# Optimization experiments

Hardware: AMD Instinct MI355X
Metric: run time of the kernel (lower is better)

Reference implementation:

```python
import jax, jax.numpy as jnp
import numpy as np

TEMPERATURE = 1.0
N_NODES = 50000
N_EDGES = 1600000
BATCH = 2
C_IN = 64
C_OUT = 64


def setup_inputs() -> dict:
    key = jax.random.key(0)
    k = jax.random.split(key, 8)
    # edge_index with no self-loops: tgt = (src + 1 + off) % N, off in [0, N-2)
    src = jax.random.randint(k[0], (N_EDGES,), 0, N_NODES, dtype=jnp.int64)
    off = jax.random.randint(k[1], (N_EDGES,), 0, N_NODES - 1, dtype=jnp.int64)
    tgt = (src + 1 + off) % N_NODES
    edge_index = jnp.stack([src, tgt])  # (2, E)
    x = jax.random.normal(k[2], (BATCH, N_NODES, C_IN), dtype=jnp.float32)
    f_disc_orig = jax.random.uniform(k[3], (N_EDGES,), dtype=jnp.float32)
    fluxes = jax.random.normal(k[4], (BATCH, N_NODES), dtype=jnp.float32)
    W_conc = jax.random.normal(k[5], (C_OUT, C_IN), dtype=jnp.float32) * (1.0 / np.sqrt(C_IN))
    W_disc = jax.random.normal(k[6], (C_OUT, C_IN), dtype=jnp.float32) * (1.0 / np.sqrt(C_IN))
    bias = jnp.zeros((C_OUT,), dtype=jnp.float32)
    return {"x": x, "edge_index": edge_index, "f_disc_orig": f_disc_orig,
            "fluxes": fluxes, "W_conc": W_conc, "W_disc": W_disc, "bias": bias}


def reference(x, edge_index, f_disc_orig, fluxes, W_conc, W_disc, bias):
    B, N, _ = x.shape
    src0, tgt0 = edge_index[0], edge_index[1]  # original edges (no self-loops)
    loops = jnp.arange(N, dtype=edge_index.dtype)
    src = jnp.concatenate([src0, loops])  # (E+N,)
    tgt = jnp.concatenate([tgt0, loops])
    # GCN symmetric normalization D^{-1/2} A D^{-1/2} (with self-loops)
    deg = jnp.zeros((N,), x.dtype).at[tgt].add(1.0)
    dis = jnp.where(deg > 0, jax.lax.rsqrt(jnp.maximum(deg, 1e-30)), 0.0)
    norm = dis[src] * dis[tgt]  # (E+N,)
    # dynamic discordant strength on original (non-self-loop) edges
    sign_prod = jnp.tanh(fluxes[:, src0] * fluxes[:, tgt0] / TEMPERATURE)  # (B, E)
    keep = (1.0 + sign_prod) * 0.5
    fdo = f_disc_orig[None, :]
    f_disc = keep * fdo + (1.0 - keep) * (1.0 - fdo)  # (B, E)
    # self-loop messages are purely concordant (f_disc = 0)
    f_full = jnp.concatenate([f_disc, jnp.zeros((B, N), x.dtype)], axis=1)  # (B, E+N)
    # transform once per node, then gather per edge
    xc = jnp.einsum('bni,oi->bno', x, W_conc)  # (B, N, O)
    xd = jnp.einsum('bni,oi->bno', x, W_disc)
    msg = norm[None, :, None] * ((1.0 - f_full)[..., None] * xc[:, src] +
                                 f_full[..., None] * xd[:, src])  # (B, E+N, O)
    out = jnp.zeros((B, N, xc.shape[-1]), x.dtype).at[:, tgt].add(msg)
    return out + bias
```

## Files before the change

### kernel.cpp

```cpp
#include <hip/hip_runtime.h>
#include <math.h>


constexpr int C = 64;
constexpr int CNB = 512;
constexpr int CCAP = 18432;

typedef short short8 __attribute__((ext_vector_type(8)));
typedef float f32x4 __attribute__((ext_vector_type(4)));

__device__ __forceinline__ unsigned pack_bf16x2(float a, float b) {
    unsigned ua = __float_as_uint(a);
    ua = (ua + 0x7fffu + ((ua >> 16) & 1u)) >> 16;
    unsigned ub = __float_as_uint(b);
    ub = (ub + 0x7fffu + ((ub >> 16) & 1u)) >> 16;
    return ua | (ub << 16);
}
__device__ __forceinline__ float bflo(unsigned p) { return __uint_as_float(p << 16); }
__device__ __forceinline__ float bfhi(unsigned p) { return __uint_as_float(p & 0xffff0000u); }

__global__ __launch_bounds__(256) void convert_kernel(
    const float* __restrict__ x, unsigned* __restrict__ xb2, int nwords) {
    int i = blockIdx.x * blockDim.x + threadIdx.x;
    int stride = gridDim.x * blockDim.x;
    const float2* x2 = (const float2*)x;
    for (int w = i; w < nwords; w += stride) {
        float2 xv = x2[w];
        xb2[w] = pack_bf16x2(xv.x, xv.y);
    }
}

__global__ __launch_bounds__(256) void binA1_kernel(
    const int* __restrict__ src, const int* __restrict__ tgt,
    const float* __restrict__ fdo, int* __restrict__ coarseCursor,
    unsigned long long* __restrict__ slab, int E, int ncoarse) {
    __shared__ int hcnt[128];
    __shared__ int hbase[128];
    const int tid = threadIdx.x;
    const int chunk0 = blockIdx.x * 4096;
    if (tid < 128) hcnt[tid] = 0;
    __syncthreads();
#pragma unroll
    for (int k = 0; k < 16; ++k) {
        int e = chunk0 + tid + k * 256;
        if (e < E) atomicAdd(&hcnt[tgt[e] >> 9], 1);
    }
    __syncthreads();
    if (tid < ncoarse) {
        int c = hcnt[tid];
        hbase[tid] = c ? atomicAdd(&coarseCursor[tid], c) : 0;
        hcnt[tid] = 0;
    }
    __syncthreads();
#pragma unroll
    for (int k = 0; k < 16; ++k) {
        int e = chunk0 + tid + k * 256;
        if (e < E) {
            int t = tgt[e];
            int b = t >> 9;
            int pos = hbase[b] + atomicAdd(&hcnt[b], 1);
            if (pos < CCAP) {
                unsigned q = (unsigned)(fdo[e] * 32767.0f + 0.5f);
                unsigned long long en = (unsigned long long)(unsigned)src[e]
                                      | ((unsigned long long)(unsigned)(t & 511) << 17)
                                      | ((unsigned long long)q << 26);
                slab[(size_t)b * CCAP + pos] = en;
            }
        }
    }
}

__global__ __launch_bounds__(1024) void binA2_kernel(
    const unsigned long long* __restrict__ slab,
    const int* __restrict__ coarseCursor, const float* __restrict__ flux,
    unsigned* __restrict__ epackFine, float4* __restrict__ nodeinfo,
    int N, int ncoarse) {
    const int b = blockIdx.x;
    const int tid = threadIdx.x;
    __shared__ int ncnt[CNB];
    __shared__ int nsc[CNB];
    __shared__ int ncur[CNB];
    int cnt = min(coarseCursor[b], CCAP);
    if (tid < CNB) { ncnt[tid] = 0; ncur[tid] = 0; }
    __syncthreads();
    const unsigned long long* sl = slab + (size_t)b * CCAP;
    for (int i = tid; i < cnt; i += 1024)
        atomicAdd(&ncnt[(int)((sl[i] >> 17) & 511)], 1);
    __syncthreads();
    if (tid < CNB) nsc[tid] = ncnt[tid];
    __syncthreads();
    for (int off = 1; off < CNB; off <<= 1) {
        int v = (tid < CNB && tid >= off) ? nsc[tid - off] : 0;
        __syncthreads();
        if (tid < CNB) nsc[tid] += v;
        __syncthreads();
    }
    for (int i = tid; i < cnt; i += 1024) {
        unsigned long long e = sl[i];
        int s = (int)(e & 0x1FFFFull);
        int tl = (int)((e >> 17) & 511);
        unsigned q = (unsigned)((e >> 26) & 0x7FFF);
        int pos = nsc[tl] - ncnt[tl] + atomicAdd(&ncur[tl], 1);
        epackFine[(size_t)b * CCAP + pos] = (unsigned)s | (q << 17);
    }
    if (tid < CNB) {
        int n = b * CNB + tid;
        if (n < N) {
            int dg = ncnt[tid];
            int rs = b * CCAP + (nsc[tid] - dg);
            float4 ni;
            ni.x = rsqrtf((float)(dg + 1));
            ni.y = flux[n];
            ni.z = flux[N + n];
            ni.w = __int_as_float((dg << 21) | rs);
            nodeinfo[n] = ni;
        }
    }
}

__global__ __launch_bounds__(256) void aggregate_kernel(
    const float4* __restrict__ nodeinfo, const unsigned* __restrict__ epackFine,
    const unsigned* __restrict__ xb2, unsigned* __restrict__ up,
    unsigned* __restrict__ vp, int N) {
    const int lane = threadIdx.x & 63;
    const int wslot = threadIdx.x >> 6;
    const int node = blockIdx.x * 4 + wslot;
    __shared__ float4 s_e[4][2][64];
    if (node >= N) return;
    const int g = lane >> 5;
    const int hl = lane & 31;
    float4 ni = nodeinfo[node];
    const unsigned wbits = (unsigned)__float_as_int(ni.w);
    const int start = (int)(wbits & 0x1FFFFFu);
    const int end = start + (int)(wbits >> 21);
    const float dt = ni.x, f0t = ni.y, f1t = ni.z;
    const char* xbg = (const char*)xb2 + (size_t)g * N * 128 + hl * 4;
    float ux = 0.f, uy = 0.f, vx = 0.f, vy = 0.f;
    for (int base = start; base < end; base += 64) {
        int cnt64 = min(64, end - base);
        if (lane < cnt64) {
            unsigned p = epackFine[base + lane];
            int s = (int)(p & 0x1FFFFu);
            float fd = (float)(p >> 17) * (1.0f / 32767.0f);
            float4 nis = nodeinfo[s];
            float nrm = nis.x * dt;
            float p0 = nis.y * f0t;
            float p1 = nis.z * f1t;
            float k0 = 1.0f / (1.0f + __expf(-2.0f * p0));
            float k1 = 1.0f / (1.0f + __expf(-2.0f * p1));
            float w = 2.0f * fd - 1.0f;
            float f0 = fmaf(k0, w, 1.0f - fd);
            float f1 = fmaf(k1, w, 1.0f - fd);
            float soff = __int_as_float(s << 7);
            s_e[wslot][0][lane] = make_float4(soff, nrm * (1.0f - f0), nrm * f0, 0.f);
            s_e[wslot][1][lane] = make_float4(soff, nrm * (1.0f - f1), nrm * f1, 0.f);
        }
        float4 r = s_e[wslot][g][0];
        unsigned xpN = *(const unsigned*)(xbg + __float_as_int(r.x));
        float ccN = r.y, cdN = r.z;
        for (int j = 1; j < cnt64; ++j) {
            unsigned xp = xpN;
            float cc = ccN, cd = cdN;
            float4 r2 = s_e[wslot][g][j];
            xpN = *(const unsigned*)(xbg + __float_as_int(r2.x));
            ccN = r2.y; cdN = r2.z;
            float x0 = bflo(xp), x1 = bfhi(xp);
            ux = fmaf(cc, x0, ux); uy = fmaf(cc, x1, uy);
            vx = fmaf(cd, x0, vx); vy = fmaf(cd, x1, vy);
        }
        float x0 = bflo(xpN), x1 = bfhi(xpN);
        ux = fmaf(ccN, x0, ux); uy = fmaf(ccN, x1, uy);
        vx = fmaf(cdN, x0, vx); vy = fmaf(cdN, x1, vy);
    }
    unsigned xs = *(const unsigned*)(xbg + ((size_t)node << 7));
    float d2 = dt * dt;
    ux = fmaf(d2, bflo(xs), ux);
    uy = fmaf(d2, bfhi(xs), uy);
    size_t o32 = ((size_t)(g * N + node)) * 32 + hl;
    up[o32] = pack_bf16x2(ux, uy);
    vp[o32] = pack_bf16x2(vx, vy);
}

__device__ __forceinline__ short8 make_bfrag(const float* __restrict__ row, int off) {
    const float4* p = (const float4*)(row + off);
    float4 lo = p[0], hi = p[1];
    uint4 w;
    w.x = pack_bf16x2(lo.x, lo.y);
    w.y = pack_bf16x2(lo.z, lo.w);
    w.z = pack_bf16x2(hi.x, hi.y);
    w.w = pack_bf16x2(hi.z, hi.w);
    return __builtin_bit_cast(short8, w);
}

__global__ __launch_bounds__(256) void gemm_mfma_kernel(
    const unsigned* __restrict__ up, const unsigned* __restrict__ vp,
    const float* __restrict__ Wc, const float* __restrict__ Wd,
    const float* __restrict__ bias, float* __restrict__ out, int ntiles) {
    const int lane = threadIdx.x & 63;
    const int nl = lane & 15;
    const int quad = lane >> 4;
    const int wave = blockIdx.x * 4 + (threadIdx.x >> 6);
    const int nwaves = gridDim.x * 4;

    short8 bf[4][4];
    float bt[4];
#pragma unroll
    for (int t = 0; t < 4; ++t) {
        int n = 16 * t + nl;
        const float* wcr = Wc + n * 64;
        const float* wdr = Wd + n * 64;
        bf[0][t] = make_bfrag(wcr, quad * 8);
        bf[1][t] = make_bfrag(wcr, 32 + quad * 8);
        bf[2][t] = make_bfrag(wdr, quad * 8);
        bf[3][t] = make_bfrag(wdr, 32 + quad * 8);
        bt[t] = bias[n];
    }

    for (int tile = wave; tile < ntiles; tile += nwaves) {
        int row = tile * 16 + nl;
        const uint4* ur = (const uint4*)(up + (size_t)row * 32);
        const uint4* vr = (const uint4*)(vp + (size_t)row * 32);
        short8 a0 = __builtin_bit_cast(short8, ur[quad]);
        short8 a1 = __builtin_bit_cast(short8, ur[4 + quad]);
        short8 a2 = __builtin_bit_cast(short8, vr[quad]);
        short8 a3 = __builtin_bit_cast(short8, vr[4 + quad]);
        f32x4 acc[4];
#pragma unroll
        for (int t = 0; t < 4; ++t) {
            f32x4 z = {0.f, 0.f, 0.f, 0.f};
            acc[t] = __builtin_amdgcn_mfma_f32_16x16x32_bf16(a0, bf[0][t], z, 0, 0, 0);
            acc[t] = __builtin_amdgcn_mfma_f32_16x16x32_bf16(a1, bf[1][t], acc[t], 0, 0, 0);
            acc[t] = __builtin_amdgcn_mfma_f32_16x16x32_bf16(a2, bf[2][t], acc[t], 0, 0, 0);
            acc[t] = __builtin_amdgcn_mfma_f32_16x16x32_bf16(a3, bf[3][t], acc[t], 0, 0, 0);
        }
        float* ob = out + ((size_t)(tile * 16 + quad * 4) << 6);
#pragma unroll
        for (int t = 0; t < 4; ++t) {
            int col = 16 * t + nl;
#pragma unroll
            for (int r = 0; r < 4; ++r)
                ob[(r << 6) + col] = acc[t][r] + bt[t];
        }
    }
}

extern "C" void kernel_launch(void* const* d_in, const int* in_sizes, int n_in,
                              void* d_out, int out_size, void* d_ws, size_t ws_size,
                              hipStream_t stream) {
    const float* x = (const float*)d_in[0];
    const int* ei = (const int*)d_in[1];
    const float* fdo = (const float*)d_in[2];
    const float* flux = (const float*)d_in[3];
    const float* Wc = (const float*)d_in[4];
    const float* Wd = (const float*)d_in[5];
    const float* bias = (const float*)d_in[6];
    float* out = (float*)d_out;

    const int E = in_sizes[2];
    const int BN = in_sizes[3];
    const int N = BN / 2;
    const int ncoarse = (N + CNB - 1) / CNB;

    auto align = [](size_t o) { return (o + 255) & ~(size_t)255; };
    char* ws = (char*)d_ws;
    size_t o = 0;
    int* coarseCursor = (int*)(ws + o);
    size_t zero_end = align((size_t)ncoarse * 4);
    o = zero_end;
    float4* nodeinfo = (float4*)(ws + o);          o = align(o + (size_t)N * 16);
    unsigned long long* slab = (unsigned long long*)(ws + o);
    unsigned* up = (unsigned*)slab;
    o = align(o + (size_t)ncoarse * CCAP * 8);
    unsigned* epackFine = (unsigned*)(ws + o);     o = align(o + (size_t)ncoarse * CCAP * 4);
    unsigned* xb2 = (unsigned*)(ws + o);           o = align(o + (size_t)BN * 32 * 4);
    unsigned* vp = (unsigned*)(ws + o);            o += (size_t)BN * 32 * 4;

    const int* srcp = ei;
    const int* tgtp = ei + E;

    hipMemsetAsync(coarseCursor, 0, zero_end, stream);
    convert_kernel<<<2048, 256, 0, stream>>>(x, xb2, BN * 32);
    binA1_kernel<<<(E + 4095) / 4096, 256, 0, stream>>>(srcp, tgtp, fdo,
                                                        coarseCursor, slab, E, ncoarse);
    binA2_kernel<<<ncoarse, 1024, 0, stream>>>(slab, coarseCursor, flux,
                                               epackFine, nodeinfo, N, ncoarse);
    aggregate_kernel<<<(N + 3) / 4, 256, 0, stream>>>(nodeinfo, epackFine, xb2,
                                                      up, vp, N);
    gemm_mfma_kernel<<<512, 256, 0, stream>>>(up, vp, Wc, Wd, bias, out, BN / 16);
}
```

Before: 221.9 us.

## Widen aggregate gathers to 16B per lane, shrink coarse bins, fold memset

The aggregate kernel now processes four edges at a time per wavefront. Each 16-lane group loads 16-byte bf16 chunks of a source row, and the partial sums are reduced with cross-lane shuffles. This replaces 4-byte per-lane gathers, cutting the number of memory instructions and the length of the serial edge loop. Coarse bins shrink from 512 to 128 nodes, which gives more binA2 blocks, and binA1 handles larger chunks with a larger shared histogram. The cursor memset is folded into the convert kernel, but convert and binA1 both modify coarseCursor and ordering between them relies on stream order. CCAP=5120 for 128 nodes gives less per-bin headroom and risks overflow with skewed degrees.

New measurement: 220.7 us. Within noise of the previous version (-0.5%).

```diff
diff --git a/kernel.cpp b/kernel.cpp
--- a/kernel.cpp
+++ b/kernel.cpp
@@ -3,8 +3,8 @@
 
 
 constexpr int C = 64;
-constexpr int CNB = 512;
-constexpr int CCAP = 18432;
+constexpr int CNB = 128;
+constexpr int CCAP = 5120;
 
 typedef short short8 __attribute__((ext_vector_type(8)));
 typedef float f32x4 __attribute__((ext_vector_type(4)));
@@ -20,8 +20,10 @@
 __device__ __forceinline__ float bfhi(unsigned p) { return __uint_as_float(p & 0xffff0000u); }
 
 __global__ __launch_bounds__(256) void convert_kernel(
-    const float* __restrict__ x, unsigned* __restrict__ xb2, int nwords) {
+    const float* __restrict__ x, unsigned* __restrict__ xb2, int nwords,
+    int* __restrict__ coarseCursor, int ncoarse) {
     int i = blockIdx.x * blockDim.x + threadIdx.x;
+    if (i < ncoarse) coarseCursor[i] = 0;
     int stride = gridDim.x * blockDim.x;
     const float2* x2 = (const float2*)x;
     for (int w = i; w < nwords; w += stride) {
@@ -34,36 +36,36 @@
     const int* __restrict__ src, const int* __restrict__ tgt,
     const float* __restrict__ fdo, int* __restrict__ coarseCursor,
     unsigned long long* __restrict__ slab, int E, int ncoarse) {
-    __shared__ int hcnt[128];
-    __shared__ int hbase[128];
+    __shared__ int hcnt[512];
+    __shared__ int hbase[512];
     const int tid = threadIdx.x;
-    const int chunk0 = blockIdx.x * 4096;
-    if (tid < 128) hcnt[tid] = 0;
-    __syncthreads();
-#pragma unroll
-    for (int k = 0; k < 16; ++k) {
+    const int chunk0 = blockIdx.x * 8192;
+    for (int c = tid; c < 512; c += 256) hcnt[c] = 0;
+    __syncthreads();
+#pragma unroll 4
+    for (int k = 0; k < 32; ++k) {
         int e = chunk0 + tid + k * 256;
-        if (e < E) atomicAdd(&hcnt[tgt[e] >> 9], 1);
-    }
-    __syncthreads();
-    if (tid < ncoarse) {
-        int c = hcnt[tid];
-        hbase[tid] = c ? atomicAdd(&coarseCursor[tid], c) : 0;
-        hcnt[tid] = 0;
-    }
-    __syncthreads();
-#pragma unroll
-    for (int k = 0; k < 16; ++k) {
+        if (e < E) atomicAdd(&hcnt[tgt[e] >> 7], 1);
+    }
+    __syncthreads();
+    for (int c = tid; c < ncoarse; c += 256) {
+        int cc = hcnt[c];
+        hbase[c] = cc ? atomicAdd(&coarseCursor[c], cc) : 0;
+        hcnt[c] = 0;
+    }
+    __syncthreads();
+#pragma unroll 4
+    for (int k = 0; k < 32; ++k) {
         int e = chunk0 + tid + k * 256;
         if (e < E) {
             int t = tgt[e];
-            int b = t >> 9;
+            int b = t >> 7;
             int pos = hbase[b] + atomicAdd(&hcnt[b], 1);
             if (pos < CCAP) {
                 unsigned q = (unsigned)(fdo[e] * 32767.0f + 0.5f);
                 unsigned long long en = (unsigned long long)(unsigned)src[e]
-                                      | ((unsigned long long)(unsigned)(t & 511) << 17)
-                                      | ((unsigned long long)q << 26);
+                                      | ((unsigned long long)(unsigned)(t & 127) << 17)
+                                      | ((unsigned long long)q << 24);
                 slab[(size_t)b * CCAP + pos] = en;
             }
         }
@@ -73,8 +75,7 @@
 __global__ __launch_bounds__(1024) void binA2_kernel(
     const unsigned long long* __restrict__ slab,
     const int* __restrict__ coarseCursor, const float* __restrict__ flux,
-    unsigned* __restrict__ epackFine, float4* __restrict__ nodeinfo,
-    int N, int ncoarse) {
+    unsigned* __restrict__ epackFine, float4* __restrict__ nodeinfo, int N) {
     const int b = blockIdx.x;
     const int tid = threadIdx.x;
     __shared__ int ncnt[CNB];
@@ -85,7 +86,7 @@
     __syncthreads();
     const unsigned long long* sl = slab + (size_t)b * CCAP;
     for (int i = tid; i < cnt; i += 1024)
-        atomicAdd(&ncnt[(int)((sl[i] >> 17) & 511)], 1);
+        atomicAdd(&ncnt[(int)((sl[i] >> 17) & 127)], 1);
     __syncthreads();
     if (tid < CNB) nsc[tid] = ncnt[tid];
     __syncthreads();
@@ -98,8 +99,8 @@
     for (int i = tid; i < cnt; i += 1024) {
         unsigned long long e = sl[i];
         int s = (int)(e & 0x1FFFFull);
-        int tl = (int)((e >> 17) & 511);
-        unsigned q = (unsigned)((e >> 26) & 0x7FFF);
+        int tl = (int)((e >> 17) & 127);
+        unsigned q = (unsigned)((e >> 24) & 0x7FFF);
         int pos = nsc[tl] - ncnt[tl] + atomicAdd(&ncur[tl], 1);
         epackFine[(size_t)b * CCAP + pos] = (unsigned)s | (q << 17);
     }
@@ -127,21 +128,25 @@
     const int node = blockIdx.x * 4 + wslot;
     __shared__ float4 s_e[4][2][64];
     if (node >= N) return;
-    const int g = lane >> 5;
-    const int hl = lane & 31;
+    const int e2 = lane >> 4;
+    const int q16 = lane & 15;
+    const int g = q16 >> 3;
+    const int p = q16 & 7;
     float4 ni = nodeinfo[node];
     const unsigned wbits = (unsigned)__float_as_int(ni.w);
     const int start = (int)(wbits & 0x1FFFFFu);
     const int end = start + (int)(wbits >> 21);
     const float dt = ni.x, f0t = ni.y, f1t = ni.z;
-    const char* xbg = (const char*)xb2 + (size_t)g * N * 128 + hl * 4;
-    float ux = 0.f, uy = 0.f, vx = 0.f, vy = 0.f;
+    const char* xbg = (const char*)xb2 + (size_t)g * N * 128 + p * 16;
+    float au[8] = {0, 0, 0, 0, 0, 0, 0, 0};
+    float av[8] = {0, 0, 0, 0, 0, 0, 0, 0};
     for (int base = start; base < end; base += 64) {
-        int cnt64 = min(64, end - base);
-        if (lane < cnt64) {
-            unsigned p = epackFine[base + lane];
-            int s = (int)(p & 0x1FFFFu);
-            float fd = (float)(p >> 17) * (1.0f / 32767.0f);
+        int cnt = min(64, end - base);
+        int cntp = (cnt + 3) & ~3;
+        if (lane < cnt) {
+            unsigned pe = epackFine[base + lane];
+            int s = (int)(pe & 0x1FFFFu);
+            float fd = (float)(pe >> 17) * (1.0f / 32767.0f);
             float4 nis = nodeinfo[s];
             float nrm = nis.x * dt;
             float p0 = nis.y * f0t;
@@ -154,31 +159,69 @@
             float soff = __int_as_float(s << 7);
             s_e[wslot][0][lane] = make_float4(soff, nrm * (1.0f - f0), nrm * f0, 0.f);
             s_e[wslot][1][lane] = make_float4(soff, nrm * (1.0f - f1), nrm * f1, 0.f);
-        }
-        float4 r = s_e[wslot][g][0];
-        unsigned xpN = *(const unsigned*)(xbg + __float_as_int(r.x));
-        float ccN = r.y, cdN = r.z;
-        for (int j = 1; j < cnt64; ++j) {
-            unsigned xp = xpN;
+        } else if (lane < cntp) {
+            float4 z = make_float4(0.f, 0.f, 0.f, 0.f);
+            s_e[wslot][0][lane] = z;
+            s_e[wslot][1][lane] = z;
+        }
+        float4 r0 = s_e[wslot][g][e2];
+        uint4 xwN = *(const uint4*)(xbg + __float_as_int(r0.x));
+        float ccN = r0.y, cdN = r0.z;
+        for (int j = 4; j < cntp; j += 4) {
+            uint4 xw = xwN;
             float cc = ccN, cd = cdN;
-            float4 r2 = s_e[wslot][g][j];
-            xpN = *(const unsigned*)(xbg + __float_as_int(r2.x));
+            float4 r2 = s_e[wslot][g][j + e2];
+            xwN = *(const uint4*)(xbg + __float_as_int(r2.x));
             ccN = r2.y; cdN = r2.z;
-            float x0 = bflo(xp), x1 = bfhi(xp);
-            ux = fmaf(cc, x0, ux); uy = fmaf(cc, x1, uy);
-            vx = fmaf(cd, x0, vx); vy = fmaf(cd, x1, vy);
-        }
-        float x0 = bflo(xpN), x1 = bfhi(xpN);
-        ux = fmaf(ccN, x0, ux); uy = fmaf(ccN, x1, uy);
-        vx = fmaf(cdN, x0, vx); vy = fmaf(cdN, x1, vy);
-    }
-    unsigned xs = *(const unsigned*)(xbg + ((size_t)node << 7));
-    float d2 = dt * dt;
-    ux = fmaf(d2, bflo(xs), ux);
-    uy = fmaf(d2, bfhi(xs), uy);
-    size_t o32 = ((size_t)(g * N + node)) * 32 + hl;
-    up[o32] = pack_bf16x2(ux, uy);
-    vp[o32] = pack_bf16x2(vx, vy);
+#pragma unroll
+            for (int w = 0; w < 4; ++w) {
+                unsigned xp = (&xw.x)[w];
+                float lo = bflo(xp), hi = bfhi(xp);
+                au[2 * w] = fmaf(cc, lo, au[2 * w]);
+                au[2 * w + 1] = fmaf(cc, hi, au[2 * w + 1]);
+                av[2 * w] = fmaf(cd, lo, av[2 * w]);
+                av[2 * w + 1] = fmaf(cd, hi, av[2 * w + 1]);
+            }
+        }
+#pragma unroll
+        for (int w = 0; w < 4; ++w) {
+            unsigned xp = (&xwN.x)[w];
+            float lo = bflo(xp), hi = bfhi(xp);
+            au[2 * w] = fmaf(ccN, lo, au[2 * w]);
+            au[2 * w + 1] = fmaf(ccN, hi, au[2 * w + 1]);
+            av[2 * w] = fmaf(cdN, lo, av[2 * w]);
+            av[2 * w + 1] = fmaf(cdN, hi, av[2 * w + 1]);
+        }
+    }
+#pragma unroll
+    for (int k = 0; k < 8; ++k) {
+        au[k] += __shfl_xor(au[k], 16, 64);
+        au[k] += __shfl_xor(au[k], 32, 64);
+        av[k] += __shfl_xor(av[k], 16, 64);
+        av[k] += __shfl_xor(av[k], 32, 64);
+    }
+    if (e2 == 0) {
+        uint4 xs = *(const uint4*)(xbg + ((size_t)node << 7));
+        float d2 = dt * dt;
+#pragma unroll
+        for (int w = 0; w < 4; ++w) {
+            unsigned xp = (&xs.x)[w];
+            au[2 * w] = fmaf(d2, bflo(xp), au[2 * w]);
+            au[2 * w + 1] = fmaf(d2, bfhi(xp), au[2 * w + 1]);
+        }
+        uint4 uo, vo;
+        uo.x = pack_bf16x2(au[0], au[1]);
+        uo.y = pack_bf16x2(au[2], au[3]);
+        uo.z = pack_bf16x2(au[4], au[5]);
+        uo.w = pack_bf16x2(au[6], au[7]);
+        vo.x = pack_bf16x2(av[0], av[1]);
+        vo.y = pack_bf16x2(av[2], av[3]);
+        vo.z = pack_bf16x2(av[4], av[5]);
+        vo.w = pack_bf16x2(av[6], av[7]);
+        size_t wo = ((size_t)(g * N + node)) * 32 + 4 * p;
+        *(uint4*)(up + wo) = uo;
+        *(uint4*)(vp + wo) = vo;
+    }
 }
 
 __device__ __forceinline__ short8 make_bfrag(const float* __restrict__ row, int off) {
@@ -264,9 +307,7 @@
     auto align = [](size_t o) { return (o + 255) & ~(size_t)255; };
     char* ws = (char*)d_ws;
     size_t o = 0;
-    int* coarseCursor = (int*)(ws + o);
-    size_t zero_end = align((size_t)ncoarse * 4);
-    o = zero_end;
+    int* coarseCursor = (int*)(ws + o);            o = align(o + (size_t)ncoarse * 4);
     float4* nodeinfo = (float4*)(ws + o);          o = align(o + (size_t)N * 16);
     unsigned long long* slab = (unsigned long long*)(ws + o);
     unsigned* up = (unsigned*)slab;
@@ -278,12 +319,11 @@
     const int* srcp = ei;
     const int* tgtp = ei + E;
 
-    hipMemsetAsync(coarseCursor, 0, zero_end, stream);
-    convert_kernel<<<2048, 256, 0, stream>>>(x, xb2, BN * 32);
-    binA1_kernel<<<(E + 4095) / 4096, 256, 0, stream>>>(srcp, tgtp, fdo,
+    convert_kernel<<<2048, 256, 0, stream>>>(x, xb2, BN * 32, coarseCursor, ncoarse);
+    binA1_kernel<<<(E + 8191) / 8192, 256, 0, stream>>>(srcp, tgtp, fdo,
                                                         coarseCursor, slab, E, ncoarse);
     binA2_kernel<<<ncoarse, 1024, 0, stream>>>(slab, coarseCursor, flux,
-                                               epackFine, nodeinfo, N, ncoarse);
+                                               epackFine, nodeinfo, N);
     aggregate_kernel<<<(N + 3) / 4, 256, 0, stream>>>(nodeinfo, epackFine, xb2,
                                                       up, vp, N);
     gemm_mfma_kernel<<<512, 256, 0, stream>>>(up, vp, Wc, Wd, bias, out, BN / 16);
```
